# Kernel optimization log

Hardware: AMD Instinct MI355X
Metric: run time of the kernel (lower is better)

## Reference

```python
import jax, jax.numpy as jnp
import numpy as np

H = 12            # num_heads
GRID = 14         # sqrt(num_patches)
NP_ = GRID * GRID # num_patches = 196


def _relative_position_index():
    coords = np.stack(np.meshgrid(np.arange(GRID), np.arange(GRID), indexing='ij'))  # [2,14,14]
    flat = coords.reshape(2, -1)                                   # [2,196]
    rel = flat[:, :, None] - flat[:, None, :]                      # [2,196,196]
    rel = rel.transpose(1, 2, 0).astype(np.int32)                  # [196,196,2]
    rel[..., 0] += GRID - 1
    rel[..., 1] += GRID - 1
    rel[..., 0] *= 2 * GRID - 1
    return rel.sum(-1)                                             # [196,196] in [0,729)


def setup_inputs() -> dict:
    key = jax.random.key(0)
    k1, k2, k3, k4 = jax.random.split(key, 4)
    B, N, C = 64, NP_ + 1, 768
    return {
        'x': jax.random.normal(k1, (B, N, C), dtype=jnp.float32),
        'w_qkv': jax.random.normal(k2, (3 * C, C), dtype=jnp.float32) * 0.02,
        'w_proj': jax.random.normal(k3, (C, C), dtype=jnp.float32) * 0.02,
        'b_proj': jnp.zeros((C,), dtype=jnp.float32),
        # torch inits the table to zeros; use small randn so the bias path is exercised
        'rpb_table': jax.random.normal(k4, ((2 * GRID - 1) ** 2, H), dtype=jnp.float32) * 0.02,
        'rel_idx': jnp.asarray(_relative_position_index()),
    }


def reference(x, w_qkv, w_proj, b_proj, rpb_table, rel_idx):
    B, N, C = x.shape
    hd = C // H
    scale = hd ** -0.5
    qkv = (x @ w_qkv.T).reshape(B, N, 3, H, hd).transpose(2, 0, 3, 1, 4)  # [3,B,H,N,hd]
    q, k, v = qkv[0] * scale, qkv[1], qkv[2]
    attn = jnp.einsum('bhqd,bhkd->bhqk', q, k)                            # [B,H,N,N]
    bias = rpb_table[rel_idx.reshape(-1)].reshape(NP_, NP_, H).transpose(2, 0, 1)  # [H,196,196]
    attn = attn.at[:, :, 1:, 1:].add(bias[None])                          # skip CLS row/col
    attn = jax.nn.softmax(attn, axis=-1)
    out = jnp.einsum('bhqk,bhkd->bqhd', attn, v).reshape(B, N, C)
    return out @ w_proj.T + b_proj
```

## Files before the change

kernel.cpp:

```cpp
#include <hip/hip_runtime.h>

typedef float f32x4 __attribute__((ext_vector_type(4)));
typedef short short8 __attribute__((ext_vector_type(8)));

#define DEVI static __device__ __forceinline__

DEVI ushort f2bf(float f) {
  unsigned u = __builtin_bit_cast(unsigned, f);
  u += 0x7fffu + ((u >> 16) & 1u);
  return (ushort)(u >> 16);
}

DEVI short8 pack8(float4 a, float4 b) {
  union { ushort u[8]; short8 v; } t;
  t.u[0] = f2bf(a.x); t.u[1] = f2bf(a.y); t.u[2] = f2bf(a.z); t.u[3] = f2bf(a.w);
  t.u[4] = f2bf(b.x); t.u[5] = f2bf(b.y); t.u[6] = f2bf(b.z); t.u[7] = f2bf(b.w);
  return t.v;
}

DEVI f32x4 MFMA16(short8 a, short8 b, f32x4 c) {
  return __builtin_amdgcn_mfma_f32_16x16x32_bf16(a, b, c, 0, 0, 0);
}

DEVI void gld16(const ushort* g, ushort* l) {
  __builtin_amdgcn_global_load_lds(
      (const __attribute__((address_space(1))) unsigned int*)g,
      (__attribute__((address_space(3))) unsigned int*)l, 16, 0, 0);
}

__global__ void prep_all(const float* __restrict__ table, const int* __restrict__ rel_idx,
                         float* __restrict__ bias,
                         const float* __restrict__ x, ushort* __restrict__ xbf,
                         const float* __restrict__ wq, ushort* __restrict__ wqb,
                         const float* __restrict__ wp, ushort* __restrict__ wpb) {
  const int bid = blockIdx.x, tid = threadIdx.x;
  if (bid < 2028) {
    int i = bid * 256 + tid;
    int k = i % 208;
    int t = i / 208;
    int q = t % 208;
    int h = t / 208;
    float v;
    if (k >= 197) v = -1e30f;
    else if (q == 0 || k == 0 || q >= 197) v = 0.0f;
    else v = table[rel_idx[(q - 1) * 196 + (k - 1)] * 12 + h];
    bias[i] = v;
  } else if (bid < 6756) {
    int i = (bid - 2028) * 256 + tid;
    float4 a = ((const float4*)x)[i * 2];
    float4 b = ((const float4*)x)[i * 2 + 1];
    ((short8*)xbf)[i] = pack8(a, b);
  } else if (bid < 7620) {
    int i = (bid - 6756) * 256 + tid;
    float4 a = ((const float4*)wq)[i * 2];
    float4 b = ((const float4*)wq)[i * 2 + 1];
    ((short8*)wqb)[i] = pack8(a, b);
  } else {
    int i = (bid - 7620) * 256 + tid;
    float4 a = ((const float4*)wp)[i * 2];
    float4 b = ((const float4*)wp)[i * 2 + 1];
    ((short8*)wpb)[i] = pack8(a, b);
  }
}

template <int MODE, int NBN>
__launch_bounds__(256, 3)
__global__ void gemm128(const ushort* __restrict__ A, const ushort* __restrict__ B,
                        ushort* __restrict__ q, ushort* __restrict__ k,
                        ushort* __restrict__ v,
                        const float* __restrict__ bprj, float* __restrict__ out) {
  __shared__ __align__(16) ushort As[3][4096];
  __shared__ __align__(16) ushort Bs[3][4096];

  const int tid = threadIdx.x;
  const int lane = tid & 63, wid = tid >> 6;
  const int wm = wid >> 1, wn = wid & 1;
  const int l15 = lane & 15, l4 = lane >> 4;

  const int nwg = gridDim.x;
  const int qc = nwg >> 3, rc = nwg & 7;
  const int xcd = blockIdx.x & 7, sub = blockIdx.x >> 3;
  const int wgid = (xcd < rc ? xcd * (qc + 1) : rc * (qc + 1) + (xcd - rc) * qc) + sub;
  const int bn = wgid % NBN, bm = wgid / NBN;

  const int c0 = wid * 2, c1 = wid * 2 + 1;
  const int r0 = c0 * 16 + (lane >> 2);
  const int r1 = c1 * 16 + (lane >> 2);
  const int g = lane & 3;
  const int col0 = (g << 3) ^ ((r0 & 6) << 2);
  const int col1 = (g << 3) ^ ((r1 & 6) << 2);
  long ar0 = bm * 128 + r0; if (ar0 > 12607) ar0 = 12607;
  long ar1 = bm * 128 + r1; if (ar1 > 12607) ar1 = 12607;
  const ushort* pA0 = A + ar0 * 768 + col0;
  const ushort* pA1 = A + ar1 * 768 + col1;
  const ushort* pB0 = B + (size_t)(bn * 128 + r0) * 768 + col0;
  const ushort* pB1 = B + (size_t)(bn * 128 + r1) * 768 + col1;

  const int xk = (l4 * 8) ^ ((l15 & 6) << 2);
  int aoff[4], boff[4];
#pragma unroll
  for (int m = 0; m < 4; m++) aoff[m] = (wm * 64 + m * 16 + l15) * 32 + xk;
#pragma unroll
  for (int n = 0; n < 4; n++) boff[n] = (wn * 64 + n * 16 + l15) * 32 + xk;

  f32x4 acc[4][4];
#pragma unroll
  for (int m = 0; m < 4; m++)
#pragma unroll
    for (int n = 0; n < 4; n++) acc[m][n] = (f32x4)0.0f;

#define STAGE(SL, KO)                           \
  gld16(pA0 + (KO), &As[SL][c0 * 512]);         \
  gld16(pA1 + (KO), &As[SL][c1 * 512]);         \
  gld16(pB0 + (KO), &Bs[SL][c0 * 512]);         \
  gld16(pB1 + (KO), &Bs[SL][c1 * 512]);

#define COMPUTE(SL)                                                 \
  {                                                                 \
    short8 af[4], bv[4];                                            \
    _Pragma("unroll") for (int m = 0; m < 4; m++)                   \
        af[m] = *(const short8*)&As[SL][aoff[m]];                   \
    _Pragma("unroll") for (int n = 0; n < 4; n++)                   \
        bv[n] = *(const short8*)&Bs[SL][boff[n]];                   \
    __builtin_amdgcn_s_setprio(1);                                  \
    _Pragma("unroll") for (int m = 0; m < 4; m++)                   \
        _Pragma("unroll") for (int n = 0; n < 4; n++)               \
            acc[m][n] = MFMA16(af[m], bv[n], acc[m][n]);            \
    __builtin_amdgcn_s_setprio(0);                                  \
  }

  STAGE(0, 0)
  STAGE(1, 32)

  int sl_c = 0, sl_s = 2;
  for (int t = 0; t < 22; ++t) {
    asm volatile("s_waitcnt vmcnt(4)" ::: "memory");
    asm volatile("s_waitcnt lgkmcnt(0)" ::: "memory");
    __builtin_amdgcn_s_barrier();
    __builtin_amdgcn_sched_barrier(0);
    STAGE(sl_s, (t + 2) * 32)
    COMPUTE(sl_c)
    sl_c = (sl_c == 2) ? 0 : sl_c + 1;
    sl_s = (sl_s == 2) ? 0 : sl_s + 1;
  }
  asm volatile("s_waitcnt vmcnt(4)" ::: "memory");
  asm volatile("s_waitcnt lgkmcnt(0)" ::: "memory");
  __builtin_amdgcn_s_barrier();
  __builtin_amdgcn_sched_barrier(0);
  COMPUTE(1)
  asm volatile("s_waitcnt vmcnt(0)" ::: "memory");
  asm volatile("s_waitcnt lgkmcnt(0)" ::: "memory");
  __builtin_amdgcn_s_barrier();
  __builtin_amdgcn_sched_barrier(0);
  COMPUTE(2)

  if (MODE == 0) {
    const int s = bn / 6;
    ushort* dst = (s == 0) ? q : ((s == 1) ? k : v);
    const float qs = (s == 0) ? 0.125f : 1.0f;
    const int cbase = bn * 128 + wn * 64 - s * 768;
    const int hh = cbase >> 6;
#pragma unroll
    for (int m = 0; m < 4; m++) {
#pragma unroll
      for (int r = 0; r < 4; r++) {
        int gm = bm * 128 + wm * 64 + m * 16 + l4 * 4 + r;
        if (gm >= 12608) continue;
        int b = gm / 197;
        int ns = gm - b * 197;
        size_t base = (size_t)((b * 12 + hh) * 197 + ns) * 64;
#pragma unroll
        for (int n = 0; n < 4; n++)
          dst[base + n * 16 + l15] = f2bf(acc[m][n][r] * qs);
      }
    }
  } else {
    float bb[4];
#pragma unroll
    for (int n = 0; n < 4; n++) bb[n] = bprj[bn * 128 + wn * 64 + n * 16 + l15];
#pragma unroll
    for (int m = 0; m < 4; m++) {
#pragma unroll
      for (int r = 0; r < 4; r++) {
        int gm = bm * 128 + wm * 64 + m * 16 + l4 * 4 + r;
        if (gm >= 12608) continue;
#pragma unroll
        for (int n = 0; n < 4; n++)
          out[(size_t)gm * 768 + bn * 128 + wn * 64 + n * 16 + l15] = acc[m][n][r] + bb[n];
      }
    }
  }
#undef STAGE
#undef COMPUTE
}

__launch_bounds__(512)
__global__ void attn(const ushort* __restrict__ qws, const ushort* __restrict__ kws,
                     const ushort* __restrict__ vws, const float* __restrict__ biasws,
                     ushort* __restrict__ aout) {
  __shared__ __align__(16) ushort Ks[208 * 72];
  __shared__ __align__(16) ushort Vt[64 * 232];
  __shared__ __align__(16) ushort Ps[8 * 16 * 232];

  const int bh = blockIdx.x;
  const int b = bh / 12;
  const int h = bh - b * 12;
  const ushort* qb = qws + (size_t)bh * 197 * 64;
  const ushort* kb = kws + (size_t)bh * 197 * 64;
  const ushort* vb = vws + (size_t)bh * 197 * 64;

  const int tid = threadIdx.x;
  const int lane = tid & 63, wid = tid >> 6;
  const int l15 = lane & 15, l4 = lane >> 4;

  for (int c = tid; c < 208 * 8; c += 512) {
    int n = c >> 3, col = (c & 7) << 3;
    short8 v = (short8)0;
    if (n < 197) v = *(const short8*)(kb + n * 64 + col);
    *(short8*)&Ks[n * 72 + col] = v;
  }
  for (int c = tid; c < 224 * 8; c += 512) {
    int n = c % 224;
    int d0 = (c / 224) << 3;
    ushort tmp[8] = {0, 0, 0, 0, 0, 0, 0, 0};
    if (n < 197) {
      short8 v = *(const short8*)(vb + n * 64 + d0);
#pragma unroll
      for (int j = 0; j < 8; j++) tmp[j] = (ushort)v[j];
    }
#pragma unroll
    for (int j = 0; j < 8; j++) Vt[(d0 + j) * 232 + n] = tmp[j];
  }
  __syncthreads();

  ushort* pb = &Ps[wid * (16 * 232)];
  const float* biasb = biasws + (size_t)h * 208 * 208;

  for (int t = wid; t < 13; t += 8) {
    const int q0 = t * 16;
    int qr = q0 + l15; if (qr > 196) qr = 196;
    short8 aq0 = *(const short8*)(qb + qr * 64 + (l4 << 3));
    short8 aq1 = *(const short8*)(qb + qr * 64 + 32 + (l4 << 3));

    f32x4 sc[13];
    __builtin_amdgcn_s_setprio(1);
#pragma unroll
    for (int ct = 0; ct < 13; ct++) {
      short8 b0 = *(const short8*)&Ks[(ct * 16 + l15) * 72 + (l4 << 3)];
      short8 b1 = *(const short8*)&Ks[(ct * 16 + l15) * 72 + 32 + (l4 << 3)];
      f32x4 s = (f32x4)0.0f;
      s = MFMA16(aq0, b0, s);
      s = MFMA16(aq1, b1, s);
      sc[ct] = s;
    }
    __builtin_amdgcn_s_setprio(0);

    float mx[4] = {-1e38f, -1e38f, -1e38f, -1e38f};
#pragma unroll
    for (int ct = 0; ct < 13; ct++) {
#pragma unroll
      for (int r = 0; r < 4; r++) {
        float bv = biasb[(q0 + l4 * 4 + r) * 208 + ct * 16 + l15];
        float v = sc[ct][r] + bv;
        sc[ct][r] = v;
        mx[r] = fmaxf(mx[r], v);
      }
    }
#pragma unroll
    for (int r = 0; r < 4; r++) {
      mx[r] = fmaxf(mx[r], __shfl_xor(mx[r], 1));
      mx[r] = fmaxf(mx[r], __shfl_xor(mx[r], 2));
      mx[r] = fmaxf(mx[r], __shfl_xor(mx[r], 4));
      mx[r] = fmaxf(mx[r], __shfl_xor(mx[r], 8));
    }
    float sum[4] = {0.f, 0.f, 0.f, 0.f};
#pragma unroll
    for (int ct = 0; ct < 13; ct++) {
#pragma unroll
      for (int r = 0; r < 4; r++) {
        float p = __expf(sc[ct][r] - mx[r]);
        sc[ct][r] = p;
        sum[r] += p;
      }
    }
#pragma unroll
    for (int r = 0; r < 4; r++) {
      sum[r] += __shfl_xor(sum[r], 1);
      sum[r] += __shfl_xor(sum[r], 2);
      sum[r] += __shfl_xor(sum[r], 4);
      sum[r] += __shfl_xor(sum[r], 8);
    }

#pragma unroll
    for (int ct = 0; ct < 13; ct++)
#pragma unroll
      for (int r = 0; r < 4; r++)
        pb[(l4 * 4 + r) * 232 + ct * 16 + l15] = f2bf(sc[ct][r]);
#pragma unroll
    for (int r = 0; r < 4; r++)
      pb[(l4 * 4 + r) * 232 + 208 + l15] = 0;

    short8 pa[7];
#pragma unroll
    for (int kk = 0; kk < 7; kk++)
      pa[kk] = *(const short8*)&pb[l15 * 232 + kk * 32 + (l4 << 3)];
    f32x4 o[4];
    __builtin_amdgcn_s_setprio(1);
#pragma unroll
    for (int dt = 0; dt < 4; dt++) {
      f32x4 acc = (f32x4)0.0f;
#pragma unroll
      for (int kk = 0; kk < 7; kk++) {
        short8 bv = *(const short8*)&Vt[(dt * 16 + l15) * 232 + kk * 32 + (l4 << 3)];
        acc = MFMA16(pa[kk], bv, acc);
      }
      o[dt] = acc;
    }
    __builtin_amdgcn_s_setprio(0);

    float rs[4];
#pragma unroll
    for (int r = 0; r < 4; r++) rs[r] = 1.0f / sum[r];
#pragma unroll
    for (int dt = 0; dt < 4; dt++) {
#pragma unroll
      for (int r = 0; r < 4; r++) {
        int row = q0 + l4 * 4 + r;
        if (row < 197) {
          float v = o[dt][r] * rs[r];
          aout[(size_t)(b * 197 + row) * 768 + h * 64 + dt * 16 + l15] = f2bf(v);
        }
      }
    }
  }
}

extern "C" void kernel_launch(void* const* d_in, const int* in_sizes, int n_in,
                              void* d_out, int out_size, void* d_ws, size_t ws_size,
                              hipStream_t stream) {
  const float* x      = (const float*)d_in[0];
  const float* w_qkv  = (const float*)d_in[1];
  const float* w_proj = (const float*)d_in[2];
  const float* b_proj = (const float*)d_in[3];
  const float* rpb    = (const float*)d_in[4];
  const int*   relidx = (const int*)d_in[5];
  float* out = (float*)d_out;

  char* ws = (char*)d_ws;
  const size_t HB = (size_t)12608 * 768 * 2;
  ushort* xbf   = (ushort*)(ws);
  ushort* qws   = (ushort*)(ws + HB);
  ushort* kws   = (ushort*)(ws + 2 * HB);
  ushort* vws   = (ushort*)(ws + 3 * HB);
  float*  bias  = (float*)(ws + 4 * HB);
  ushort* wqkvb = (ushort*)(ws + 4 * HB + 2076672);
  ushort* wprjb = (ushort*)(ws + 4 * HB + 2076672 + 3538944);
  ushort* aout  = xbf;

  hipLaunchKernelGGL(prep_all, dim3(7908), dim3(256), 0, stream,
                     rpb, relidx, bias, x, xbf, w_qkv, wqkvb, w_proj, wprjb);
  hipLaunchKernelGGL((gemm128<0, 18>), dim3(18 * 99), dim3(256), 0, stream,
                     xbf, wqkvb, qws, kws, vws, nullptr, nullptr);
  hipLaunchKernelGGL(attn, dim3(768), dim3(512), 0, stream, qws, kws, vws, bias, aout);
  hipLaunchKernelGGL((gemm128<1, 6>), dim3(6 * 99), dim3(256), 0, stream,
                     aout, wprjb, nullptr, nullptr, nullptr, b_proj, out);
}
```

Measured before the change: 145.1 us.

## Replace 128x128 GEMM with 256x256 8-wave ping-pong pipelined kernel

Swaps the 128x128, 4-wave triple-buffered GEMM for a 256x256 tile GEMM with 8 waves. It uses 64-wide K slices, double buffering and an 8-phase schedule that interleaves half-tile global loads with MFMA phases under barriers. The larger tiles raise reuse per loaded byte and cut the number of workgroups. In exchange, QKV gets 450 workgroups and proj only 150 on a 256-CU device, which underfills the proj launch, and the per-phase barriers add sync cost.

```diff
diff --git a/kernel.cpp b/kernel.cpp
--- a/kernel.cpp
+++ b/kernel.cpp
@@ -63,18 +63,22 @@
   }
 }
 
+#define BARRIER() { asm volatile("" ::: "memory"); __builtin_amdgcn_s_barrier(); asm volatile("" ::: "memory"); }
+#define VMC(N) asm volatile("s_waitcnt vmcnt(" #N ")" ::: "memory")
+#define NOP
+
 template <int MODE, int NBN>
-__launch_bounds__(256, 3)
-__global__ void gemm128(const ushort* __restrict__ A, const ushort* __restrict__ B,
-                        ushort* __restrict__ q, ushort* __restrict__ k,
-                        ushort* __restrict__ v,
-                        const float* __restrict__ bprj, float* __restrict__ out) {
-  __shared__ __align__(16) ushort As[3][4096];
-  __shared__ __align__(16) ushort Bs[3][4096];
+__launch_bounds__(512, 2)
+__global__ void gemm8p(const ushort* __restrict__ A, const ushort* __restrict__ B,
+                       ushort* __restrict__ q, ushort* __restrict__ k,
+                       ushort* __restrict__ v,
+                       const float* __restrict__ bprj, float* __restrict__ out) {
+  __shared__ __align__(16) ushort AS[32768];
+  __shared__ __align__(16) ushort BS[32768];
 
   const int tid = threadIdx.x;
   const int lane = tid & 63, wid = tid >> 6;
-  const int wm = wid >> 1, wn = wid & 1;
+  const int wm = wid >> 2, wn = wid & 3;
   const int l15 = lane & 15, l4 = lane >> 4;
 
   const int nwg = gridDim.x;
@@ -83,115 +87,119 @@
   const int wgid = (xcd < rc ? xcd * (qc + 1) : rc * (qc + 1) + (xcd - rc) * qc) + sub;
   const int bn = wgid % NBN, bm = wgid / NBN;
 
-  const int c0 = wid * 2, c1 = wid * 2 + 1;
-  const int r0 = c0 * 16 + (lane >> 2);
-  const int r1 = c1 * 16 + (lane >> 2);
-  const int g = lane & 3;
-  const int col0 = (g << 3) ^ ((r0 & 6) << 2);
-  const int col1 = (g << 3) ^ ((r1 & 6) << 2);
-  long ar0 = bm * 128 + r0; if (ar0 > 12607) ar0 = 12607;
-  long ar1 = bm * 128 + r1; if (ar1 > 12607) ar1 = 12607;
-  const ushort* pA0 = A + ar0 * 768 + col0;
-  const ushort* pA1 = A + ar1 * 768 + col1;
-  const ushort* pB0 = B + (size_t)(bn * 128 + r0) * 768 + col0;
-  const ushort* pB1 = B + (size_t)(bn * 128 + r1) * 768 + col1;
-
-  const int xk = (l4 * 8) ^ ((l15 & 6) << 2);
-  int aoff[4], boff[4];
-#pragma unroll
-  for (int m = 0; m < 4; m++) aoff[m] = (wm * 64 + m * 16 + l15) * 32 + xk;
-#pragma unroll
-  for (int n = 0; n < 4; n++) boff[n] = (wn * 64 + n * 16 + l15) * 32 + xk;
-
-  f32x4 acc[4][4];
-#pragma unroll
-  for (int m = 0; m < 4; m++)
+  const int lr = lane >> 3;
+  const int cg = lane & 7;
+  const ushort* pa[2][2];
+  const ushort* pb[2][2];
+#pragma unroll
+  for (int h = 0; h < 2; h++) {
+#pragma unroll
+    for (int j = 0; j < 2; j++) {
+      int rhl = wid * 8 + lr + j * 64;
+      int scol = (cg ^ (rhl & 7)) * 8;
+      long garow = (long)bm * 256 + (rhl >> 4) * 32 + h * 16 + (rhl & 15);
+      if (garow > 12607) garow = 12607;
+      pa[h][j] = A + garow * 768 + scol;
+      pb[h][j] = B + ((long)bn * 256 + h * 128 + rhl) * 768 + scol;
+    }
+  }
+
+  const int cs0 = (l4 * 8) ^ ((l15 & 7) << 3);
+
+  f32x4 acc[8][4];
+#pragma unroll
+  for (int m = 0; m < 8; m++)
 #pragma unroll
     for (int n = 0; n < 4; n++) acc[m][n] = (f32x4)0.0f;
 
-#define STAGE(SL, KO)                           \
-  gld16(pA0 + (KO), &As[SL][c0 * 512]);         \
-  gld16(pA1 + (KO), &As[SL][c1 * 512]);         \
-  gld16(pB0 + (KO), &Bs[SL][c0 * 512]);         \
-  gld16(pB1 + (KO), &Bs[SL][c1 * 512]);
-
-#define COMPUTE(SL)                                                 \
-  {                                                                 \
-    short8 af[4], bv[4];                                            \
-    _Pragma("unroll") for (int m = 0; m < 4; m++)                   \
-        af[m] = *(const short8*)&As[SL][aoff[m]];                   \
-    _Pragma("unroll") for (int n = 0; n < 4; n++)                   \
-        bv[n] = *(const short8*)&Bs[SL][boff[n]];                   \
-    __builtin_amdgcn_s_setprio(1);                                  \
-    _Pragma("unroll") for (int m = 0; m < 4; m++)                   \
-        _Pragma("unroll") for (int n = 0; n < 4; n++)               \
-            acc[m][n] = MFMA16(af[m], bv[n], acc[m][n]);            \
-    __builtin_amdgcn_s_setprio(0);                                  \
-  }
-
-  STAGE(0, 0)
-  STAGE(1, 32)
-
-  int sl_c = 0, sl_s = 2;
-  for (int t = 0; t < 22; ++t) {
-    asm volatile("s_waitcnt vmcnt(4)" ::: "memory");
-    asm volatile("s_waitcnt lgkmcnt(0)" ::: "memory");
-    __builtin_amdgcn_s_barrier();
-    __builtin_amdgcn_sched_barrier(0);
-    STAGE(sl_s, (t + 2) * 32)
-    COMPUTE(sl_c)
-    sl_c = (sl_c == 2) ? 0 : sl_c + 1;
-    sl_s = (sl_s == 2) ? 0 : sl_s + 1;
-  }
-  asm volatile("s_waitcnt vmcnt(4)" ::: "memory");
-  asm volatile("s_waitcnt lgkmcnt(0)" ::: "memory");
-  __builtin_amdgcn_s_barrier();
-  __builtin_amdgcn_sched_barrier(0);
-  COMPUTE(1)
-  asm volatile("s_waitcnt vmcnt(0)" ::: "memory");
-  asm volatile("s_waitcnt lgkmcnt(0)" ::: "memory");
-  __builtin_amdgcn_s_barrier();
-  __builtin_amdgcn_sched_barrier(0);
-  COMPUTE(2)
+#define SA(BUF, H, KT) { gld16(pa[H][0] + (KT) * 64, AS + (BUF) * 16384 + (H) * 8192 + wid * 512);        \
+                         gld16(pa[H][1] + (KT) * 64, AS + (BUF) * 16384 + (H) * 8192 + wid * 512 + 4096); }
+#define SB(BUF, H, KT) { gld16(pb[H][0] + (KT) * 64, BS + (BUF) * 16384 + (H) * 8192 + wid * 512);        \
+                         gld16(pb[H][1] + (KT) * 64, BS + (BUF) * 16384 + (H) * 8192 + wid * 512 + 4096); }
+
+#define PHASE(BUF, FH, KK, STG, WAITC)                                                        \
+  {                                                                                           \
+    short8 af[4], bv[4];                                                                      \
+    const int cko = cs0 ^ ((KK) << 5);                                                        \
+    _Pragma("unroll") for (int j = 0; j < 4; j++)                                             \
+      af[j] = *(const short8*)&AS[(BUF) * 16384 + (FH) * 8192 + (wm * 4 + j) * 1024 +         \
+                                  l15 * 64 + cko];                                            \
+    _Pragma("unroll") for (int n = 0; n < 4; n++)                                             \
+      bv[n] = *(const short8*)&BS[(BUF) * 16384 + (wn >> 1) * 8192 +                          \
+                                  ((wn & 1) * 64 + n * 16 + l15) * 64 + cko];                 \
+    STG;                                                                                      \
+    WAITC;                                                                                    \
+    BARRIER();                                                                                \
+    __builtin_amdgcn_s_setprio(1);                                                            \
+    _Pragma("unroll") for (int j = 0; j < 4; j++)                                             \
+      _Pragma("unroll") for (int n = 0; n < 4; n++)                                           \
+        acc[(FH) + 2 * j][n] = MFMA16(af[j], bv[n], acc[(FH) + 2 * j][n]);                    \
+    __builtin_amdgcn_s_setprio(0);                                                            \
+    BARRIER();                                                                                \
+  }
+
+  SA(0, 0, 0) SA(0, 1, 0) SB(0, 0, 0) SB(0, 1, 0) SA(1, 0, 1)
+  VMC(2);
+  BARRIER();
+
+  for (int i = 0; i < 5; ++i) {
+    const int t1 = 2 * i + 1, t2 = 2 * i + 2, t3 = 2 * i + 3;
+    PHASE(0, 0, 0, SA(1, 1, t1), NOP)
+    PHASE(0, 1, 0, SB(1, 0, t1), NOP)
+    PHASE(0, 0, 1, SB(1, 1, t1), NOP)
+    PHASE(0, 1, 1, SA(0, 0, t2), VMC(2))
+    PHASE(1, 0, 0, SA(0, 1, t2), NOP)
+    PHASE(1, 1, 0, SB(0, 0, t2), NOP)
+    PHASE(1, 0, 1, SB(0, 1, t2), NOP)
+    PHASE(1, 1, 1, SA(1, 0, t3), VMC(2))
+  }
+  PHASE(0, 0, 0, SA(1, 1, 11), NOP)
+  PHASE(0, 1, 0, SB(1, 0, 11), NOP)
+  PHASE(0, 0, 1, SB(1, 1, 11), NOP)
+  PHASE(0, 1, 1, NOP, VMC(0))
+  PHASE(1, 0, 0, NOP, NOP)
+  PHASE(1, 1, 0, NOP, NOP)
+  PHASE(1, 0, 1, NOP, NOP)
+  PHASE(1, 1, 1, NOP, NOP)
 
   if (MODE == 0) {
-    const int s = bn / 6;
+    const int c6 = (bn * 256 + wn * 64) >> 6;
+    const int s = c6 / 12, hh = c6 % 12;
     ushort* dst = (s == 0) ? q : ((s == 1) ? k : v);
     const float qs = (s == 0) ? 0.125f : 1.0f;
-    const int cbase = bn * 128 + wn * 64 - s * 768;
-    const int hh = cbase >> 6;
-#pragma unroll
-    for (int m = 0; m < 4; m++) {
-#pragma unroll
-      for (int r = 0; r < 4; r++) {
-        int gm = bm * 128 + wm * 64 + m * 16 + l4 * 4 + r;
+#pragma unroll
+    for (int f = 0; f < 8; f++) {
+#pragma unroll
+      for (int r = 0; r < 4; r++) {
+        int gm = bm * 256 + wm * 128 + f * 16 + l4 * 4 + r;
         if (gm >= 12608) continue;
         int b = gm / 197;
         int ns = gm - b * 197;
         size_t base = (size_t)((b * 12 + hh) * 197 + ns) * 64;
 #pragma unroll
         for (int n = 0; n < 4; n++)
-          dst[base + n * 16 + l15] = f2bf(acc[m][n][r] * qs);
+          dst[base + n * 16 + l15] = f2bf(acc[f][n][r] * qs);
       }
     }
   } else {
     float bb[4];
 #pragma unroll
-    for (int n = 0; n < 4; n++) bb[n] = bprj[bn * 128 + wn * 64 + n * 16 + l15];
-#pragma unroll
-    for (int m = 0; m < 4; m++) {
-#pragma unroll
-      for (int r = 0; r < 4; r++) {
-        int gm = bm * 128 + wm * 64 + m * 16 + l4 * 4 + r;
+    for (int n = 0; n < 4; n++) bb[n] = bprj[bn * 256 + wn * 64 + n * 16 + l15];
+#pragma unroll
+    for (int f = 0; f < 8; f++) {
+#pragma unroll
+      for (int r = 0; r < 4; r++) {
+        int gm = bm * 256 + wm * 128 + f * 16 + l4 * 4 + r;
         if (gm >= 12608) continue;
 #pragma unroll
         for (int n = 0; n < 4; n++)
-          out[(size_t)gm * 768 + bn * 128 + wn * 64 + n * 16 + l15] = acc[m][n][r] + bb[n];
-      }
-    }
-  }
-#undef STAGE
-#undef COMPUTE
+          out[(size_t)gm * 768 + bn * 256 + wn * 64 + n * 16 + l15] = acc[f][n][r] + bb[n];
+      }
+    }
+  }
+#undef SA
+#undef SB
+#undef PHASE
 }
 
 __launch_bounds__(512)
@@ -359,9 +367,9 @@
 
   hipLaunchKernelGGL(prep_all, dim3(7908), dim3(256), 0, stream,
                      rpb, relidx, bias, x, xbf, w_qkv, wqkvb, w_proj, wprjb);
-  hipLaunchKernelGGL((gemm128<0, 18>), dim3(18 * 99), dim3(256), 0, stream,
+  hipLaunchKernelGGL((gemm8p<0, 9>), dim3(9 * 50), dim3(512), 0, stream,
                      xbf, wqkvb, qws, kws, vws, nullptr, nullptr);
   hipLaunchKernelGGL(attn, dim3(768), dim3(512), 0, stream, qws, kws, vws, bias, aout);
-  hipLaunchKernelGGL((gemm128<1, 6>), dim3(6 * 99), dim3(256), 0, stream,
+  hipLaunchKernelGGL((gemm8p<1, 3>), dim3(3 * 50), dim3(512), 0, stream,
                      aout, wprjb, nullptr, nullptr, nullptr, b_proj, out);
 }
```

New measurement: 147.7 us. Within noise of the previous version (+1.8%).

## Use 256x256 tiles with 512 threads for QKV GEMM, double-buffer proj GEMM

Applied to the files above, without the earlier changes.

The QKV projection GEMM moves from 128x128 tiles with 256 threads to a dedicated 256x256-tile kernel with 512 threads, 8 waves and a 64-wide K step. Staging is double-buffered in 128 KB of LDS with an XOR swizzle. This raises arithmetic intensity and cuts the grid from 1782 to 450 workgroups, at the cost of occupancy and a tail wave. The output projection becomes its own kernel and switches from triple to double buffering with a full vmcnt(0) wait, which may expose load latency but allows 4 workgroups per CU.

```diff
diff --git a/kernel.cpp b/kernel.cpp
--- a/kernel.cpp
+++ b/kernel.cpp
@@ -27,6 +27,9 @@
       (const __attribute__((address_space(1))) unsigned int*)g,
       (__attribute__((address_space(3))) unsigned int*)l, 16, 0, 0);
 }
+
+#define VMC0() asm volatile("s_waitcnt vmcnt(0)" ::: "memory")
+#define LGK0() asm volatile("s_waitcnt lgkmcnt(0)" ::: "memory")
 
 __global__ void prep_all(const float* __restrict__ table, const int* __restrict__ rel_idx,
                          float* __restrict__ bias,
@@ -63,18 +66,17 @@
   }
 }
 
-template <int MODE, int NBN>
-__launch_bounds__(256, 3)
-__global__ void gemm128(const ushort* __restrict__ A, const ushort* __restrict__ B,
-                        ushort* __restrict__ q, ushort* __restrict__ k,
-                        ushort* __restrict__ v,
-                        const float* __restrict__ bprj, float* __restrict__ out) {
-  __shared__ __align__(16) ushort As[3][4096];
-  __shared__ __align__(16) ushort Bs[3][4096];
+template <int NBN>
+__launch_bounds__(512)
+__global__ void qkv256(const ushort* __restrict__ A, const ushort* __restrict__ B,
+                       ushort* __restrict__ q, ushort* __restrict__ k,
+                       ushort* __restrict__ v) {
+  __shared__ __align__(16) ushort AS[2][16384];
+  __shared__ __align__(16) ushort BS[2][16384];
 
   const int tid = threadIdx.x;
   const int lane = tid & 63, wid = tid >> 6;
-  const int wm = wid >> 1, wn = wid & 1;
+  const int wm = wid >> 2, wn = wid & 3;
   const int l15 = lane & 15, l4 = lane >> 4;
 
   const int nwg = gridDim.x;
@@ -82,6 +84,103 @@
   const int xcd = blockIdx.x & 7, sub = blockIdx.x >> 3;
   const int wgid = (xcd < rc ? xcd * (qc + 1) : rc * (qc + 1) + (xcd - rc) * qc) + sub;
   const int bn = wgid % NBN, bm = wgid / NBN;
+
+  const ushort* pa[4];
+  const ushort* pb[4];
+  int ldsoff[4];
+#pragma unroll
+  for (int j = 0; j < 4; j++) {
+    int c = wid * 4 + j;
+    int row = c * 8 + (lane >> 3);
+    int scol = ((lane & 7) ^ (row & 7)) << 3;
+    long gra = (long)bm * 256 + row;
+    if (gra > 12607) gra = 12607;
+    pa[j] = A + gra * 768 + scol;
+    pb[j] = B + ((long)bn * 256 + row) * 768 + scol;
+    ldsoff[j] = c * 512;
+  }
+
+  const int xk0 = ((l4 ^ (l15 & 7)) << 3);
+  const int xk1 = (((l4 + 4) ^ (l15 & 7)) << 3);
+
+  f32x4 acc[8][4];
+#pragma unroll
+  for (int m = 0; m < 8; m++)
+#pragma unroll
+    for (int n = 0; n < 4; n++) acc[m][n] = (f32x4)0.0f;
+
+#define STAGE(BUF, KO)                                            \
+  { _Pragma("unroll") for (int j = 0; j < 4; j++) {               \
+      gld16(pa[j] + (KO), &AS[BUF][ldsoff[j]]);                   \
+      gld16(pb[j] + (KO), &BS[BUF][ldsoff[j]]);                   \
+    } }
+
+#define COMPUTE(BUF)                                                        \
+  { _Pragma("unroll") for (int kk = 0; kk < 2; kk++) {                      \
+      const int xk = kk ? xk1 : xk0;                                        \
+      short8 af[8], bv[4];                                                  \
+      _Pragma("unroll") for (int m = 0; m < 8; m++)                         \
+        af[m] = *(const short8*)&AS[BUF][(wm * 128 + m * 16 + l15) * 64 + xk]; \
+      _Pragma("unroll") for (int n = 0; n < 4; n++)                         \
+        bv[n] = *(const short8*)&BS[BUF][(wn * 64 + n * 16 + l15) * 64 + xk];  \
+      __builtin_amdgcn_s_setprio(1);                                        \
+      _Pragma("unroll") for (int m = 0; m < 8; m++)                         \
+        _Pragma("unroll") for (int n = 0; n < 4; n++)                       \
+          acc[m][n] = MFMA16(af[m], bv[n], acc[m][n]);                      \
+      __builtin_amdgcn_s_setprio(0);                                        \
+    } }
+
+  STAGE(0, 0)
+  for (int t = 0; t < 11; ++t) {
+    VMC0(); LGK0();
+    __builtin_amdgcn_s_barrier();
+    __builtin_amdgcn_sched_barrier(0);
+    STAGE((t + 1) & 1, (t + 1) * 64)
+    COMPUTE(t & 1)
+  }
+  VMC0(); LGK0();
+  __builtin_amdgcn_s_barrier();
+  __builtin_amdgcn_sched_barrier(0);
+  COMPUTE(1)
+
+  const int c6 = (bn * 256 + wn * 64) >> 6;
+  const int s = c6 / 12, hh = c6 % 12;
+  ushort* dst = (s == 0) ? q : ((s == 1) ? k : v);
+  const float qs = (s == 0) ? 0.125f : 1.0f;
+#pragma unroll
+  for (int f = 0; f < 8; f++) {
+#pragma unroll
+    for (int r = 0; r < 4; r++) {
+      int gm = bm * 256 + wm * 128 + f * 16 + l4 * 4 + r;
+      if (gm >= 12608) continue;
+      int b = gm / 197;
+      int ns = gm - b * 197;
+      size_t base = (size_t)((b * 12 + hh) * 197 + ns) * 64;
+#pragma unroll
+      for (int n = 0; n < 4; n++)
+        dst[base + n * 16 + l15] = f2bf(acc[f][n][r] * qs);
+    }
+  }
+#undef STAGE
+#undef COMPUTE
+}
+
+__launch_bounds__(256, 4)
+__global__ void proj128(const ushort* __restrict__ A, const ushort* __restrict__ B,
+                        const float* __restrict__ bprj, float* __restrict__ out) {
+  __shared__ __align__(16) ushort As[2][4096];
+  __shared__ __align__(16) ushort Bs[2][4096];
+
+  const int tid = threadIdx.x;
+  const int lane = tid & 63, wid = tid >> 6;
+  const int wm = wid >> 1, wn = wid & 1;
+  const int l15 = lane & 15, l4 = lane >> 4;
+
+  const int nwg = gridDim.x;
+  const int qc = nwg >> 3, rc = nwg & 7;
+  const int xcd = blockIdx.x & 7, sub = blockIdx.x >> 3;
+  const int wgid = (xcd < rc ? xcd * (qc + 1) : rc * (qc + 1) + (xcd - rc) * qc) + sub;
+  const int bn = wgid % 6, bm = wgid / 6;
 
   const int c0 = wid * 2, c1 = wid * 2 + 1;
   const int r0 = c0 * 16 + (lane >> 2);
@@ -109,19 +208,19 @@
 #pragma unroll
     for (int n = 0; n < 4; n++) acc[m][n] = (f32x4)0.0f;
 
-#define STAGE(SL, KO)                           \
-  gld16(pA0 + (KO), &As[SL][c0 * 512]);         \
-  gld16(pA1 + (KO), &As[SL][c1 * 512]);         \
-  gld16(pB0 + (KO), &Bs[SL][c0 * 512]);         \
-  gld16(pB1 + (KO), &Bs[SL][c1 * 512]);
-
-#define COMPUTE(SL)                                                 \
+#define STAGE(BUF, KO)                          \
+  gld16(pA0 + (KO), &As[BUF][c0 * 512]);        \
+  gld16(pA1 + (KO), &As[BUF][c1 * 512]);        \
+  gld16(pB0 + (KO), &Bs[BUF][c0 * 512]);        \
+  gld16(pB1 + (KO), &Bs[BUF][c1 * 512]);
+
+#define COMPUTE(BUF)                                                \
   {                                                                 \
     short8 af[4], bv[4];                                            \
     _Pragma("unroll") for (int m = 0; m < 4; m++)                   \
-        af[m] = *(const short8*)&As[SL][aoff[m]];                   \
+        af[m] = *(const short8*)&As[BUF][aoff[m]];                  \
     _Pragma("unroll") for (int n = 0; n < 4; n++)                   \
-        bv[n] = *(const short8*)&Bs[SL][boff[n]];                   \
+        bv[n] = *(const short8*)&Bs[BUF][boff[n]];                  \
     __builtin_amdgcn_s_setprio(1);                                  \
     _Pragma("unroll") for (int m = 0; m < 4; m++)                   \
         _Pragma("unroll") for (int n = 0; n < 4; n++)               \
@@ -130,64 +229,30 @@
   }
 
   STAGE(0, 0)
-  STAGE(1, 32)
-
-  int sl_c = 0, sl_s = 2;
-  for (int t = 0; t < 22; ++t) {
-    asm volatile("s_waitcnt vmcnt(4)" ::: "memory");
-    asm volatile("s_waitcnt lgkmcnt(0)" ::: "memory");
+  for (int t = 0; t < 23; ++t) {
+    VMC0(); LGK0();
     __builtin_amdgcn_s_barrier();
     __builtin_amdgcn_sched_barrier(0);
-    STAGE(sl_s, (t + 2) * 32)
-    COMPUTE(sl_c)
-    sl_c = (sl_c == 2) ? 0 : sl_c + 1;
-    sl_s = (sl_s == 2) ? 0 : sl_s + 1;
-  }
-  asm volatile("s_waitcnt vmcnt(4)" ::: "memory");
-  asm volatile("s_waitcnt lgkmcnt(0)" ::: "memory");
+    STAGE((t + 1) & 1, (t + 1) * 32)
+    COMPUTE(t & 1)
+  }
+  VMC0(); LGK0();
   __builtin_amdgcn_s_barrier();
   __builtin_amdgcn_sched_barrier(0);
   COMPUTE(1)
-  asm volatile("s_waitcnt vmcnt(0)" ::: "memory");
-  asm volatile("s_waitcnt lgkmcnt(0)" ::: "memory");
-  __builtin_amdgcn_s_barrier();
-  __builtin_amdgcn_sched_barrier(0);
-  COMPUTE(2)
-
-  if (MODE == 0) {
-    const int s = bn / 6;
-    ushort* dst = (s == 0) ? q : ((s == 1) ? k : v);
-    const float qs = (s == 0) ? 0.125f : 1.0f;
-    const int cbase = bn * 128 + wn * 64 - s * 768;
-    const int hh = cbase >> 6;
-#pragma unroll
-    for (int m = 0; m < 4; m++) {
-#pragma unroll
-      for (int r = 0; r < 4; r++) {
-        int gm = bm * 128 + wm * 64 + m * 16 + l4 * 4 + r;
-        if (gm >= 12608) continue;
-        int b = gm / 197;
-        int ns = gm - b * 197;
-        size_t base = (size_t)((b * 12 + hh) * 197 + ns) * 64;
-#pragma unroll
-        for (int n = 0; n < 4; n++)
-          dst[base + n * 16 + l15] = f2bf(acc[m][n][r] * qs);
-      }
-    }
-  } else {
-    float bb[4];
-#pragma unroll
-    for (int n = 0; n < 4; n++) bb[n] = bprj[bn * 128 + wn * 64 + n * 16 + l15];
-#pragma unroll
-    for (int m = 0; m < 4; m++) {
-#pragma unroll
-      for (int r = 0; r < 4; r++) {
-        int gm = bm * 128 + wm * 64 + m * 16 + l4 * 4 + r;
-        if (gm >= 12608) continue;
-#pragma unroll
-        for (int n = 0; n < 4; n++)
-          out[(size_t)gm * 768 + bn * 128 + wn * 64 + n * 16 + l15] = acc[m][n][r] + bb[n];
-      }
+
+  float bb[4];
+#pragma unroll
+  for (int n = 0; n < 4; n++) bb[n] = bprj[bn * 128 + wn * 64 + n * 16 + l15];
+#pragma unroll
+  for (int m = 0; m < 4; m++) {
+#pragma unroll
+    for (int r = 0; r < 4; r++) {
+      int gm = bm * 128 + wm * 64 + m * 16 + l4 * 4 + r;
+      if (gm >= 12608) continue;
+#pragma unroll
+      for (int n = 0; n < 4; n++)
+        out[(size_t)gm * 768 + bn * 128 + wn * 64 + n * 16 + l15] = acc[m][n][r] + bb[n];
     }
   }
 #undef STAGE
@@ -359,9 +424,9 @@
 
   hipLaunchKernelGGL(prep_all, dim3(7908), dim3(256), 0, stream,
                      rpb, relidx, bias, x, xbf, w_qkv, wqkvb, w_proj, wprjb);
-  hipLaunchKernelGGL((gemm128<0, 18>), dim3(18 * 99), dim3(256), 0, stream,
-                     xbf, wqkvb, qws, kws, vws, nullptr, nullptr);
+  hipLaunchKernelGGL((qkv256<9>), dim3(9 * 50), dim3(512), 0, stream,
+                     xbf, wqkvb, qws, kws, vws);
   hipLaunchKernelGGL(attn, dim3(768), dim3(512), 0, stream, qws, kws, vws, bias, aout);
-  hipLaunchKernelGGL((gemm128<1, 6>), dim3(6 * 99), dim3(256), 0, stream,
-                     aout, wprjb, nullptr, nullptr, nullptr, b_proj, out);
-}
+  hipLaunchKernelGGL(proj128, dim3(6 * 99), dim3(256), 0, stream,
+                     aout, wprjb, b_proj, out);
+}
```

Result: faster. 137.2 us (-5.4%).
